# Kernel tuning notes

Measured on AMD Instinct MI355X. Metric: run time of the kernel, lower is better.

The kernel has to match this reference:

```python
import jax, jax.numpy as jnp
import numpy as np

B, T, C_IN, PL, H, W = 8, 8, 256, 64, 56, 56
NT = B * T
RED = 4
CR = PL // RED            # 16 corr feature channels
PS = 7                    # patch size -> 49 correlation channels
KK = PS * PS
EPS = 1e-5
_BN_INV = np.float32(1.0 / np.sqrt(1.0 + EPS))  # eval-mode BN, running_mean=0, running_var=1


def _bn4(x, g, b):  # x [N,C,H,W], per-channel affine (eval-mode BN)
    return x * (g * _BN_INV)[None, :, None, None] + b[None, :, None, None]


def _bn5(x, g, b):  # x [B,T,C,H,W], channel axis 2
    return x * (g * _BN_INV)[None, None, :, None, None] + b[None, None, :, None, None]


def _tconv(x, w):  # depthwise temporal conv: x [B,T,Cq,H,W], w [Cq,K], 'same' padding in T
    K = w.shape[1]
    pad = K // 2
    Tn = x.shape[1]
    xp = jnp.pad(x, ((0, 0), (pad, pad), (0, 0), (0, 0), (0, 0)))
    out = w[:, 0][None, None, :, None, None] * xp[:, 0:Tn]
    for k in range(1, K):
        out = out + w[:, k][None, None, :, None, None] * xp[:, k:k + Tn]
    return out


def _correlation(a, b):  # SpatialCorrelationSampler(kernel=1, patch=PS): a,b [N,C,h,w] -> [N,PS*PS,h,w]
    pad = PS // 2
    h, w = a.shape[2], a.shape[3]
    bp = jnp.pad(b, ((0, 0), (0, 0), (pad, pad), (pad, pad)))
    outs = [jnp.sum(a * bp[:, :, di:di + h, dj:dj + w], axis=1)
            for di in range(PS) for dj in range(PS)]
    return jnp.stack(outs, axis=1)


def setup_inputs() -> dict:
    key = jax.random.key(0)
    ks = jax.random.split(key, 24)
    r = lambda i, shape, s: jax.random.normal(ks[i], shape, dtype=jnp.float32) * s
    return {
        "x": jax.random.normal(ks[0], (NT, C_IN, H, W), dtype=jnp.float32),
        "w1": r(1, (C_IN // 4, 1), 0.3), "w3": r(2, (C_IN // 4, 3), 0.3),
        "w5": r(3, (C_IN // 4, 5), 0.3), "w7": r(4, (C_IN // 4, 7), 0.3),
        "w_conv1": r(5, (PL, C_IN), 0.05), "g1": 1.0 + r(6, (PL,), 0.1), "b1": r(7, (PL,), 0.1),
        "w_conv21": r(8, (CR, PL), 0.1), "g21": 1.0 + r(9, (CR,), 0.1), "b21": r(10, (CR,), 0.1),
        "g22": 1.0 + r(11, (KK,), 0.1), "b22": r(12, (KK,), 0.1),
        "w_conv22": r(13, (PL, KK), 0.1), "g23": 1.0 + r(14, (PL,), 0.1), "b23": r(15, (PL,), 0.1),
        "w_conv2": r(16, (PL, PL, 3, 3), 0.05), "g2": 1.0 + r(17, (PL,), 0.1), "b2": r(18, (PL,), 0.1),
        "w_conv3": r(19, (C_IN, PL), 0.05), "g3": 1.0 + r(20, (C_IN,), 0.1), "b3": r(21, (C_IN,), 0.1),
    }


def reference(x, w1, w3, w5, w7, w_conv1, g1, b1, w_conv21, g21, b21,
              g22, b22, w_conv22, g23, b23, w_conv2, g2, b2, w_conv3, g3, b3):
    residual = x  # stride=1, no downsample
    # ms_group: split channels in 4 quarters, temporal dw conv k=1/3/5/7
    xt = x.reshape(B, T, C_IN, H, W)
    q = C_IN // 4
    parts = [_tconv(xt[:, :, i * q:(i + 1) * q], w) for i, w in enumerate((w1, w3, w5, w7))]
    out = jnp.concatenate(parts, axis=2).reshape(NT, C_IN, H, W)
    # net.conv1 (1x1) + bn1 + relu
    out = jax.nn.relu(_bn4(jnp.einsum('nchw,oc->nohw', out, w_conv1), g1, b1))
    # corr_outer
    res2 = out
    yt = out.reshape(B, T, PL, H, W)
    y = jax.nn.relu(_bn5(jnp.einsum('btchw,oc->btohw', yt, w_conv21), g21, b21))  # conv21+bn21
    idx = jnp.concatenate([jnp.arange(1, T), jnp.array([T - 1])])  # next-frame shift
    y2 = y[:, idx]
    a = y.reshape(NT, CR, H, W)
    b_ = y2.reshape(NT, CR, H, W)
    corr = _correlation(a, b_) / CR                         # [NT,49,H,W]
    corr = jax.nn.relu(_bn4(corr, g22, b22))
    out2 = jax.nn.relu(_bn4(jnp.einsum('nkhw,ok->nohw', corr, w_conv22), g23, b23) + res2)
    # net.conv2 (3x3) + bn2 + relu
    out = jax.lax.conv_general_dilated(out, w_conv2, (1, 1), 'SAME',
                                       dimension_numbers=('NCHW', 'OIHW', 'NCHW'))
    out = jax.nn.relu(_bn4(out, g2, b2))
    out = out + out2
    # net.conv3 (1x1) + bn3 + residual + relu
    out = _bn4(jnp.einsum('nchw,oc->nohw', out, w_conv3), g3, b3) + residual
    return jax.nn.relu(out)
```

## Files before the change

### kernel.cpp

```cpp
#include <hip/hip_runtime.h>


#define MSC_BNI 0.9999950000374997f

typedef __attribute__((ext_vector_type(8))) short bf16x8;
typedef __attribute__((ext_vector_type(4))) float f32x4;
struct __align__(8) ush4 { unsigned short v[4]; };

static __device__ __forceinline__ float b2f(unsigned short h) {
  return __uint_as_float(((unsigned int)h) << 16);
}
static __device__ __forceinline__ unsigned short f2b(float f) {
  unsigned int u = __float_as_uint(f);
  u = u + 0x7FFFu + ((u >> 16) & 1u);
  return (unsigned short)(u >> 16);
}

__global__ __launch_bounds__(256) void k0_prep(
    const float* w1, const float* w2, const float* w3, const float* w22,
    const float* w21,
    unsigned short* Wt1f, unsigned short* Wt2f, unsigned short* Wt3f,
    unsigned short* Wt4f, unsigned short* Wt5f) {
  int idx = blockIdx.x * 256 + threadIdx.x;
  if (idx < 36864) {
    int j = idx;
    int e = j & 7;
    int lane = (j >> 3) & 63;
    int m = (j >> 9) & 3;
    int kc = (j >> 11) & 1;
    int tap = j >> 12;
    int o = m * 16 + (lane & 15);
    int c = kc * 32 + (lane >> 4) * 8 + e;
    Wt2f[j] = f2b(w2[(o * 64 + c) * 9 + tap]);
  } else if (idx < 36864 + 16384) {
    int j = idx - 36864;
    int e = j & 7;
    int lane = (j >> 3) & 63;
    int m = (j >> 9) & 15;
    int kc = j >> 13;
    int o = m * 16 + (lane & 15);
    int c = kc * 32 + (lane >> 4) * 8 + e;
    Wt3f[j] = f2b(w3[o * 64 + c]);
  } else if (idx < 36864 + 16384 + 16384) {
    int j = idx - 36864 - 16384;
    int e = j & 7;
    int lane = (j >> 3) & 63;
    int m = (j >> 9) & 3;
    int kc = j >> 11;
    int o = m * 16 + (lane & 15);
    int c = kc * 32 + (lane >> 4) * 8 + e;
    Wt1f[j] = f2b(w1[o * 256 + c]);
  } else if (idx < 36864 + 16384 + 16384 + 4096) {
    int j = idx - 36864 - 16384 - 16384;
    int e = j & 7;
    int lane = (j >> 3) & 63;
    int m = (j >> 9) & 3;
    int kc = j >> 11;
    int o = m * 16 + (lane & 15);
    int c = kc * 32 + (lane >> 4) * 8 + e;
    Wt4f[j] = (c < 49) ? f2b(w22[o * 49 + c]) : (unsigned short)0;
  } else if (idx < 36864 + 16384 + 16384 + 4096 + 1024) {
    int j = idx - 36864 - 16384 - 16384 - 4096;
    int e = j & 7;
    int lane = (j >> 3) & 63;
    int kc = j >> 9;
    int o = lane & 15;
    int c = kc * 32 + (lane >> 4) * 8 + e;
    Wt5f[j] = f2b(w21[o * 64 + c]);
  }
}

__global__ __launch_bounds__(256, 2) void k12_fused(
    const float* x, unsigned short* R2t, float* Yt,
    const unsigned short* Wt1f, const unsigned short* Wt5f,
    const float* w1, const float* w3, const float* w5, const float* w7,
    const float* g, const float* bb, const float* g21, const float* b21) {
  __shared__ unsigned short sA[8960];
  int b = blockIdx.x / 98;
  int hw0 = (blockIdx.x % 98) * 32;
  int tid = threadIdx.x;
  int l = tid & 63, wv = tid >> 6;
  int l15 = l & 15, l4 = l >> 4;
  f32x4 acc[2][4][2];
#pragma unroll
  for (int tt = 0; tt < 2; tt++)
#pragma unroll
    for (int m = 0; m < 4; m++)
#pragma unroll
      for (int nt = 0; nt < 2; nt++) acc[tt][m][nt] = (f32x4){0.f, 0.f, 0.f, 0.f};

  int colp = tid & 31;
  int cbase = tid >> 5;

  for (int kc8 = 0; kc8 < 8; kc8++) {
    int c0 = kc8 * 32;
    int q = kc8 >> 1;
#pragma unroll
    for (int p = 0; p < 4; p++) {
      int c = cbase + p * 8;
      int cq = (kc8 & 1) * 32 + c;
      float wf[7];
#pragma unroll
      for (int k = 0; k < 7; k++) wf[k] = 0.f;
      if (q == 0) { wf[3] = w1[cq]; }
      else if (q == 1) { wf[2] = w3[cq*3]; wf[3] = w3[cq*3+1]; wf[4] = w3[cq*3+2]; }
      else if (q == 2) { wf[1] = w5[cq*5]; wf[2] = w5[cq*5+1]; wf[3] = w5[cq*5+2]; wf[4] = w5[cq*5+3]; wf[5] = w5[cq*5+4]; }
      else { wf[0] = w7[cq*7]; wf[1] = w7[cq*7+1]; wf[2] = w7[cq*7+2]; wf[3] = w7[cq*7+3]; wf[4] = w7[cq*7+4]; wf[5] = w7[cq*7+5]; wf[6] = w7[cq*7+6]; }
      const float* xb = x + ((size_t)(b * 8) * 256 + c0 + c) * 3136 + hw0 + colp;
      float xin[8];
#pragma unroll
      for (int t = 0; t < 8; t++) xin[t] = xb[t * 256 * 3136];
#pragma unroll
      for (int t = 0; t < 8; t++) {
        float a = 0.f;
#pragma unroll
        for (int d = -3; d <= 3; d++) {
          int ts = t + d;
          if (ts >= 0 && ts < 8) a = fmaf(wf[d + 3], xin[ts], a);
        }
        sA[(t * 32 + colp) * 34 + c] = f2b(a);
      }
    }
    __syncthreads();
#pragma unroll
    for (int tt = 0; tt < 2; tt++) {
      int t = wv * 2 + tt;
#pragma unroll
      for (int nt = 0; nt < 2; nt++) {
        int colt = nt * 16 + l15;
        bf16x8 bfr = *(const bf16x8*)(sA + (t * 32 + colt) * 34 + l4 * 8);
#pragma unroll
        for (int m = 0; m < 4; m++) {
          bf16x8 a = *(const bf16x8*)(Wt1f + (((kc8 * 4 + m) * 64 + l) << 3));
          acc[tt][m][nt] = __builtin_amdgcn_mfma_f32_16x16x32_bf16(a, bfr, acc[tt][m][nt], 0, 0, 0);
        }
      }
    }
    __syncthreads();
  }
  unsigned short* sOutT = sA;
  for (int tt = 0; tt < 2; tt++) {
#pragma unroll
    for (int m = 0; m < 4; m++)
#pragma unroll
      for (int nt = 0; nt < 2; nt++) {
        int col = nt * 16 + l15;
#pragma unroll
        for (int r = 0; r < 4; r++) {
          int o = m * 16 + l4 * 4 + r;
          float v = fmaxf(fmaf(acc[tt][m][nt][r], g[o] * MSC_BNI, bb[o]), 0.f);
          sOutT[(wv * 32 + col) * 70 + o] = f2b(v);
        }
      }
    __syncthreads();
#pragma unroll
    for (int k = 0; k < 4; k++) {
      int ch = tid + k * 256;
      int tb = ch >> 8, col = (ch >> 3) & 31, gg = ch & 7;
      int t = tb * 2 + tt;
      bf16x8 v = *(const bf16x8*)(sOutT + (tb * 32 + col) * 70 + gg * 8);
      *(bf16x8*)(R2t + (((size_t)(b * 8 + t) * 3136) + hw0 + col) * 64 + gg * 8) = v;
    }
    {
      int t = wv * 2 + tt;
#pragma unroll
      for (int ct2 = 0; ct2 < 2; ct2++) {
        f32x4 a5 = (f32x4){0.f, 0.f, 0.f, 0.f};
#pragma unroll
        for (int kc = 0; kc < 2; kc++) {
          bf16x8 bfr = *(const bf16x8*)(sOutT + (wv * 32 + ct2 * 16 + l15) * 70 + kc * 32 + l4 * 8);
          bf16x8 a = *(const bf16x8*)(Wt5f + ((kc * 64 + l) << 3));
          a5 = __builtin_amdgcn_mfma_f32_16x16x32_bf16(a, bfr, a5, 0, 0, 0);
        }
        int hw = hw0 + ct2 * 16 + l15;
        float4 yv;
        {
          int o0 = l4 * 4;
          yv.x = fmaxf(fmaf(a5[0], g21[o0+0] * MSC_BNI, b21[o0+0]), 0.f);
          yv.y = fmaxf(fmaf(a5[1], g21[o0+1] * MSC_BNI, b21[o0+1]), 0.f);
          yv.z = fmaxf(fmaf(a5[2], g21[o0+2] * MSC_BNI, b21[o0+2]), 0.f);
          yv.w = fmaxf(fmaf(a5[3], g21[o0+3] * MSC_BNI, b21[o0+3]), 0.f);
        }
        *(float4*)(Yt + (((size_t)(b * 8 + t) * 3136) + hw) * 16 + l4 * 4) = yv;
      }
    }
    __syncthreads();
  }
}

__global__ __launch_bounds__(256, 2) void k4_corr(
    const float* Yt, unsigned short* COt, const float* g, const float* bb) {
  __shared__ float sb[10 * 62 * 20];
  int n = blockIdx.x / 14;
  int h0 = (blockIdx.x % 14) * 4;
  int t = n & 7;
  int n2 = (t < 7) ? n + 1 : n;
  const float* Yb = Yt + (size_t)n2 * 3136 * 16;
  for (int idx = threadIdx.x; idx < 2480; idx += 256) {
    int c4 = idx & 3;
    int pix = idx >> 2;
    int r = pix / 62, cl = pix - r * 62;
    int gr = h0 - 3 + r, gc = cl - 3;
    float4 v = make_float4(0.f, 0.f, 0.f, 0.f);
    if (gr >= 0 && gr < 56 && gc >= 0 && gc < 56)
      v = *(const float4*)(Yb + (gr * 56 + gc) * 16 + c4 * 4);
    *(float4*)&sb[(r * 62 + cl) * 20 + c4 * 4] = v;
  }
  __syncthreads();
  int pos = threadIdx.x;
  if (pos < 224) {
    int hl = pos / 56, wcol = pos - (pos / 56) * 56;
    const float* Ya = Yt + ((size_t)n * 3136 + (h0 + hl) * 56 + wcol) * 16;
    float4 a0 = *(const float4*)(Ya + 0);
    float4 a1 = *(const float4*)(Ya + 4);
    float4 a2 = *(const float4*)(Ya + 8);
    float4 a3 = *(const float4*)(Ya + 12);
    float corr[49];
    for (int di = 0; di < 7; di++) {
      for (int dj = 0; dj < 7; dj++) {
        const float* sp = &sb[((hl + di) * 62 + wcol + dj) * 20];
        float4 b0 = *(const float4*)(sp + 0);
        float4 b1 = *(const float4*)(sp + 4);
        float4 b2 = *(const float4*)(sp + 8);
        float4 b3 = *(const float4*)(sp + 12);
        float s = 0.f;
        s = fmaf(a0.x, b0.x, s); s = fmaf(a0.y, b0.y, s);
        s = fmaf(a0.z, b0.z, s); s = fmaf(a0.w, b0.w, s);
        s = fmaf(a1.x, b1.x, s); s = fmaf(a1.y, b1.y, s);
        s = fmaf(a1.z, b1.z, s); s = fmaf(a1.w, b1.w, s);
        s = fmaf(a2.x, b2.x, s); s = fmaf(a2.y, b2.y, s);
        s = fmaf(a2.z, b2.z, s); s = fmaf(a2.w, b2.w, s);
        s = fmaf(a3.x, b3.x, s); s = fmaf(a3.y, b3.y, s);
        s = fmaf(a3.z, b3.z, s); s = fmaf(a3.w, b3.w, s);
        int k = di * 7 + dj;
        corr[k] = fmaxf(fmaf(s * 0.0625f, g[k] * MSC_BNI, bb[k]), 0.f);
      }
    }
    unsigned short* Cp = COt + ((size_t)n * 3136 + (h0 + hl) * 56 + wcol) * 64;
#pragma unroll
    for (int gq = 0; gq < 8; gq++) {
      bf16x8 pv;
#pragma unroll
      for (int j = 0; j < 8; j++) {
        int k = gq * 8 + j;
        pv[j] = (k < 49) ? (short)f2b(corr[k]) : (short)0;
      }
      *(bf16x8*)(Cp + gq * 8) = pv;
    }
  }
}

__global__ __launch_bounds__(256, 2) void k56_mfma(
    const unsigned short* R2t, const unsigned short* COt, unsigned short* C2t,
    const unsigned short* Wt2f, const unsigned short* Wt4f,
    const float* g2, const float* b2, const float* g23, const float* b23) {
  __shared__ unsigned short sIn[22272];
  int n = blockIdx.x / 14;
  int h0 = (blockIdx.x % 14) * 4;
  const unsigned short* Rt = R2t + (size_t)n * 3136 * 64;
  for (int ch = threadIdx.x; ch < 2784; ch += 256) {
    int rc = ch >> 3;
    int cg = ch & 7;
    int row = rc / 58, col = rc - row * 58;
    int gr = h0 - 1 + row, gc = col - 1;
    bf16x8 v = (bf16x8){0, 0, 0, 0, 0, 0, 0, 0};
    if (gr >= 0 && gr < 56 && gc >= 0 && gc < 56)
      v = *(const bf16x8*)(Rt + (gr * 56 + gc) * 64 + cg * 8);
    *(bf16x8*)(sIn + rc * 64 + ((cg ^ (col & 7)) << 3)) = v;
  }
  __syncthreads();
  int l = threadIdx.x & 63;
  int wv = threadIdx.x >> 6;
  int l15 = l & 15, l4 = l >> 4;
  f32x4 acc[4][4];
#pragma unroll
  for (int m = 0; m < 4; m++)
#pragma unroll
    for (int t = 0; t < 4; t++) acc[m][t] = (f32x4){0.f, 0.f, 0.f, 0.f};

  for (int tap = 0; tap < 9; tap++) {
    int ky = tap / 3;
    int kx = tap - ky * 3;
    for (int kc = 0; kc < 2; kc++) {
      bf16x8 a[4];
#pragma unroll
      for (int m = 0; m < 4; m++)
        a[m] = *(const bf16x8*)(Wt2f + ((((tap * 2 + kc) * 4 + m) * 64 + l) << 3));
#pragma unroll
      for (int t = 0; t < 4; t++) {
        int ct = wv * 4 + t;
        int rowt = ct >> 2, col0 = (ct & 3) << 4;
        int lcol = col0 + l15 + kx;
        if (lcol > 57) lcol = 57;
        int us = ((((rowt + ky) * 58 + lcol) * 64) + kc * 32 + (l4 << 3))
                 ^ ((lcol & 7) << 3);
        bf16x8 b = *(const bf16x8*)(sIn + us);
#pragma unroll
        for (int m = 0; m < 4; m++)
          acc[m][t] = __builtin_amdgcn_mfma_f32_16x16x32_bf16(a[m], b, acc[m][t], 0, 0, 0);
      }
    }
  }

#pragma unroll
  for (int t = 0; t < 4; t++) {
    int ct = wv * 4 + t;
    int rowt = ct >> 2, col0 = (ct & 3) << 4;
    int cc = col0 + l15;
    int cc_cl = (cc < 56) ? cc : 55;
    int gbase = ((int)(n * 3136) + (h0 + rowt) * 56 + cc_cl) * 64;
    f32x4 acc2[4];
#pragma unroll
    for (int m = 0; m < 4; m++) acc2[m] = (f32x4){0.f, 0.f, 0.f, 0.f};
#pragma unroll
    for (int kc = 0; kc < 2; kc++) {
      bf16x8 bco = *(const bf16x8*)(COt + gbase + kc * 32 + l4 * 8);
#pragma unroll
      for (int m = 0; m < 4; m++) {
        bf16x8 a = *(const bf16x8*)(Wt4f + (((kc * 4 + m) * 64 + l) << 3));
        acc2[m] = __builtin_amdgcn_mfma_f32_16x16x32_bf16(a, bco, acc2[m], 0, 0, 0);
      }
    }
    if (cc < 56) {
      int rc = (rowt + 1) * 58 + cc + 1;
#pragma unroll
      for (int m = 0; m < 4; m++) {
        int cg0 = 2 * m + (l4 >> 1);
        int us = rc * 64 + ((cg0 ^ ((cc + 1) & 7)) << 3) + (l4 & 1) * 4;
        ush4 rv = *(const ush4*)(sIn + us);
        ush4 ov;
#pragma unroll
        for (int r = 0; r < 4; r++) {
          int o = m * 16 + l4 * 4 + r;
          float o2 = fmaxf(fmaf(acc2[m][r], g23[o] * MSC_BNI, b23[o]) + b2f(rv.v[r]), 0.f);
          float v = fmaxf(fmaf(acc[m][t][r], g2[o] * MSC_BNI, b2[o]), 0.f) + o2;
          ov.v[r] = f2b(v);
        }
        *(ush4*)(C2t + gbase + m * 16 + l4 * 4) = ov;
      }
    }
  }
}

__global__ __launch_bounds__(256, 3) void k7_mfma(
    const unsigned short* C2t, const float* x, float* outp,
    const unsigned short* Wt3f, const float* g, const float* bb) {
  __shared__ float sOut[64 * 68];
  int n = blockIdx.x / 49;
  int hw0 = (blockIdx.x % 49) * 64;
  int l = threadIdx.x & 63;
  int wv = threadIdx.x >> 6;
  int l15 = l & 15, l4 = l >> 4;
  f32x4 acc[4][4];
#pragma unroll
  for (int m = 0; m < 4; m++)
#pragma unroll
    for (int t = 0; t < 4; t++) acc[m][t] = (f32x4){0.f, 0.f, 0.f, 0.f};

#pragma unroll
  for (int kc = 0; kc < 2; kc++) {
    bf16x8 a[4];
#pragma unroll
    for (int m = 0; m < 4; m++)
      a[m] = *(const bf16x8*)(Wt3f + (((kc * 16 + wv * 4 + m) * 64 + l) << 3));
#pragma unroll
    for (int t = 0; t < 4; t++) {
      int colt = t * 16 + l15;
      bf16x8 b = *(const bf16x8*)(C2t + ((size_t)n * 3136 + hw0 + colt) * 64 + kc * 32 + l4 * 8);
#pragma unroll
      for (int m = 0; m < 4; m++)
        acc[m][t] = __builtin_amdgcn_mfma_f32_16x16x32_bf16(a[m], b, acc[m][t], 0, 0, 0);
    }
  }

  for (int m = 0; m < 4; m++) {
#pragma unroll
    for (int t = 0; t < 4; t++)
#pragma unroll
      for (int r = 0; r < 4; r++)
        sOut[(wv * 16 + l4 * 4 + r) * 68 + t * 16 + l15] = acc[m][t][r];
    __syncthreads();
#pragma unroll
    for (int s = 0; s < 4; s++) {
      int ro = (threadIdx.x >> 4) + s * 16;
      int o = (ro >> 4) * 64 + m * 16 + (ro & 15);
      int colq = (threadIdx.x & 15) * 4;
      float4 v = *(float4*)&sOut[ro * 68 + colq];
      int off = (n * 256 + o) * 3136 + hw0 + colq;
      float4 xv = *(const float4*)(x + off);
      float sg = g[o] * MSC_BNI, bo = bb[o];
      float4 ov;
      ov.x = fmaxf(fmaf(v.x, sg, bo) + xv.x, 0.f);
      ov.y = fmaxf(fmaf(v.y, sg, bo) + xv.y, 0.f);
      ov.z = fmaxf(fmaf(v.z, sg, bo) + xv.z, 0.f);
      ov.w = fmaxf(fmaf(v.w, sg, bo) + xv.w, 0.f);
      *(float4*)(outp + off) = ov;
    }
    __syncthreads();
  }
}

extern "C" void kernel_launch(void* const* d_in, const int* in_sizes, int n_in,
                              void* d_out, int out_size, void* d_ws, size_t ws_size,
                              hipStream_t stream) {
  const float* x        = (const float*)d_in[0];
  const float* w1       = (const float*)d_in[1];
  const float* w3       = (const float*)d_in[2];
  const float* w5       = (const float*)d_in[3];
  const float* w7       = (const float*)d_in[4];
  const float* w_conv1  = (const float*)d_in[5];
  const float* g1       = (const float*)d_in[6];
  const float* b1       = (const float*)d_in[7];
  const float* w_conv21 = (const float*)d_in[8];
  const float* g21      = (const float*)d_in[9];
  const float* b21      = (const float*)d_in[10];
  const float* g22      = (const float*)d_in[11];
  const float* b22      = (const float*)d_in[12];
  const float* w_conv22 = (const float*)d_in[13];
  const float* g23      = (const float*)d_in[14];
  const float* b23      = (const float*)d_in[15];
  const float* w_conv2  = (const float*)d_in[16];
  const float* g2       = (const float*)d_in[17];
  const float* b2       = (const float*)d_in[18];
  const float* w_conv3  = (const float*)d_in[19];
  const float* g3       = (const float*)d_in[20];
  const float* b3       = (const float*)d_in[21];

  char* ob = (char*)d_out;
  char* ws = (char*)d_ws;
  float*          Yt   = (float*)ob;
  unsigned short* COt  = (unsigned short*)(ob + 12845056);
  unsigned short* R2t  = (unsigned short*)(ob + 103563264);
  unsigned short* Wt2f = (unsigned short*)(ob + 134217728);
  unsigned short* Wt1f = (unsigned short*)(ob + 134291456);
  unsigned short* Wt4f = (unsigned short*)(ob + 134324224);
  unsigned short* Wt5f = (unsigned short*)(ob + 134332416);
  unsigned short* C2t  = (unsigned short*)ws;
  unsigned short* Wt3f = (unsigned short*)(ws + 25690112);

  k0_prep  <<<dim3(292),     dim3(256), 0, stream>>>(w_conv1, w_conv2, w_conv3, w_conv22,
                                                     w_conv21, Wt1f, Wt2f, Wt3f, Wt4f, Wt5f);
  k12_fused<<<dim3(8 * 98),  dim3(256), 0, stream>>>(x, R2t, Yt, Wt1f, Wt5f,
                                                     w1, w3, w5, w7, g1, b1, g21, b21);
  k4_corr  <<<dim3(64 * 14), dim3(256), 0, stream>>>(Yt, COt, g22, b22);
  k56_mfma <<<dim3(64 * 14), dim3(256), 0, stream>>>(R2t, COt, C2t, Wt2f, Wt4f, g2, b2, g23, b23);
  k7_mfma  <<<dim3(64 * 49), dim3(256), 0, stream>>>(C2t, x, (float*)d_out, Wt3f, g3, b3);
}
```

Measured before the change: 250.1 us.

## Double-buffer LDS and prefetch next channel chunk during MFMA in fused conv1 kernel

The fused temporal-conv plus conv1 kernel now double-buffers its LDS tile. Global loads of x and the temporal weights for chunk k+1 are issued before the MFMA loop on chunk k, and the next buffer is filled afterwards. This removes one barrier per iteration and is meant to hide global load latency behind the matrix math. In exchange, LDS use doubles (about 34KB per block) and the prefetched values add registers, which could cut occupancy below the 2 blocks/SM launch bound.

```diff
diff --git a/kernel.cpp b/kernel.cpp
--- a/kernel.cpp
+++ b/kernel.cpp
@@ -75,60 +75,81 @@
     const unsigned short* Wt1f, const unsigned short* Wt5f,
     const float* w1, const float* w3, const float* w5, const float* w7,
     const float* g, const float* bb, const float* g21, const float* b21) {
-  __shared__ unsigned short sA[8960];
+  __shared__ unsigned short lds[17408];
   int b = blockIdx.x / 98;
   int hw0 = (blockIdx.x % 98) * 32;
   int tid = threadIdx.x;
   int l = tid & 63, wv = tid >> 6;
   int l15 = l & 15, l4 = l >> 4;
-  f32x4 acc[2][4][2];
-#pragma unroll
-  for (int tt = 0; tt < 2; tt++)
-#pragma unroll
-    for (int m = 0; m < 4; m++)
-#pragma unroll
-      for (int nt = 0; nt < 2; nt++) acc[tt][m][nt] = (f32x4){0.f, 0.f, 0.f, 0.f};
-
   int colp = tid & 31;
   int cbase = tid >> 5;
+  const int tstr = 256 * 3136;
+
+  f32x4 acc[2][4][2];
+#pragma unroll
+  for (int tt = 0; tt < 2; tt++)
+#pragma unroll
+    for (int m = 0; m < 4; m++)
+#pragma unroll
+      for (int nt = 0; nt < 2; nt++) acc[tt][m][nt] = (f32x4){0.f, 0.f, 0.f, 0.f};
+
+  float xn[4][8];
+  float wfn[4][7];
+
+#pragma unroll
+  for (int p = 0; p < 4; p++) {
+    int c = cbase + p * 8;
+    const float* xb = x + ((size_t)(b * 8) * 256 + c) * 3136 + hw0 + colp;
+#pragma unroll
+    for (int t = 0; t < 8; t++) xn[p][t] = xb[t * tstr];
+#pragma unroll
+    for (int k = 0; k < 7; k++) wfn[p][k] = 0.f;
+    wfn[p][3] = w1[c];
+  }
+#pragma unroll
+  for (int p = 0; p < 4; p++) {
+    int c = cbase + p * 8;
+#pragma unroll
+    for (int t = 0; t < 8; t++) {
+      float a = 0.f;
+#pragma unroll
+      for (int d = -3; d <= 3; d++) {
+        int ts = t + d;
+        if (ts >= 0 && ts < 8) a = fmaf(wfn[p][d + 3], xn[p][ts], a);
+      }
+      lds[(t * 32 + colp) * 34 + c] = f2b(a);
+    }
+  }
 
   for (int kc8 = 0; kc8 < 8; kc8++) {
-    int c0 = kc8 * 32;
-    int q = kc8 >> 1;
-#pragma unroll
-    for (int p = 0; p < 4; p++) {
-      int c = cbase + p * 8;
-      int cq = (kc8 & 1) * 32 + c;
-      float wf[7];
-#pragma unroll
-      for (int k = 0; k < 7; k++) wf[k] = 0.f;
-      if (q == 0) { wf[3] = w1[cq]; }
-      else if (q == 1) { wf[2] = w3[cq*3]; wf[3] = w3[cq*3+1]; wf[4] = w3[cq*3+2]; }
-      else if (q == 2) { wf[1] = w5[cq*5]; wf[2] = w5[cq*5+1]; wf[3] = w5[cq*5+2]; wf[4] = w5[cq*5+3]; wf[5] = w5[cq*5+4]; }
-      else { wf[0] = w7[cq*7]; wf[1] = w7[cq*7+1]; wf[2] = w7[cq*7+2]; wf[3] = w7[cq*7+3]; wf[4] = w7[cq*7+4]; wf[5] = w7[cq*7+5]; wf[6] = w7[cq*7+6]; }
-      const float* xb = x + ((size_t)(b * 8) * 256 + c0 + c) * 3136 + hw0 + colp;
-      float xin[8];
-#pragma unroll
-      for (int t = 0; t < 8; t++) xin[t] = xb[t * 256 * 3136];
-#pragma unroll
-      for (int t = 0; t < 8; t++) {
-        float a = 0.f;
-#pragma unroll
-        for (int d = -3; d <= 3; d++) {
-          int ts = t + d;
-          if (ts >= 0 && ts < 8) a = fmaf(wf[d + 3], xin[ts], a);
-        }
-        sA[(t * 32 + colp) * 34 + c] = f2b(a);
-      }
-    }
     __syncthreads();
+    unsigned short* bufc = lds + (kc8 & 1) * 8704;
+    unsigned short* bufn = lds + ((kc8 + 1) & 1) * 8704;
+    if (kc8 < 7) {
+      int kn = kc8 + 1;
+      int qn = kn >> 1;
+#pragma unroll
+      for (int p = 0; p < 4; p++) {
+        int c = cbase + p * 8;
+        const float* xb = x + ((size_t)(b * 8) * 256 + kn * 32 + c) * 3136 + hw0 + colp;
+#pragma unroll
+        for (int t = 0; t < 8; t++) xn[p][t] = xb[t * tstr];
+        int cq = (kn & 1) * 32 + c;
+#pragma unroll
+        for (int k = 0; k < 7; k++) wfn[p][k] = 0.f;
+        if (qn == 0) { wfn[p][3] = w1[cq]; }
+        else if (qn == 1) { wfn[p][2] = w3[cq*3]; wfn[p][3] = w3[cq*3+1]; wfn[p][4] = w3[cq*3+2]; }
+        else if (qn == 2) { wfn[p][1] = w5[cq*5]; wfn[p][2] = w5[cq*5+1]; wfn[p][3] = w5[cq*5+2]; wfn[p][4] = w5[cq*5+3]; wfn[p][5] = w5[cq*5+4]; }
+        else { wfn[p][0] = w7[cq*7]; wfn[p][1] = w7[cq*7+1]; wfn[p][2] = w7[cq*7+2]; wfn[p][3] = w7[cq*7+3]; wfn[p][4] = w7[cq*7+4]; wfn[p][5] = w7[cq*7+5]; wfn[p][6] = w7[cq*7+6]; }
+      }
+    }
 #pragma unroll
     for (int tt = 0; tt < 2; tt++) {
       int t = wv * 2 + tt;
 #pragma unroll
       for (int nt = 0; nt < 2; nt++) {
         int colt = nt * 16 + l15;
-        bf16x8 bfr = *(const bf16x8*)(sA + (t * 32 + colt) * 34 + l4 * 8);
+        bf16x8 bfr = *(const bf16x8*)(bufc + (t * 32 + colt) * 34 + l4 * 8);
 #pragma unroll
         for (int m = 0; m < 4; m++) {
           bf16x8 a = *(const bf16x8*)(Wt1f + (((kc8 * 4 + m) * 64 + l) << 3));
@@ -136,9 +157,25 @@
         }
       }
     }
-    __syncthreads();
-  }
-  unsigned short* sOutT = sA;
+    if (kc8 < 7) {
+#pragma unroll
+      for (int p = 0; p < 4; p++) {
+        int c = cbase + p * 8;
+#pragma unroll
+        for (int t = 0; t < 8; t++) {
+          float a = 0.f;
+#pragma unroll
+          for (int d = -3; d <= 3; d++) {
+            int ts = t + d;
+            if (ts >= 0 && ts < 8) a = fmaf(wfn[p][d + 3], xn[p][ts], a);
+          }
+          bufn[(t * 32 + colp) * 34 + c] = f2b(a);
+        }
+      }
+    }
+  }
+  __syncthreads();
+  unsigned short* sOutT = lds;
   for (int tt = 0; tt < 2; tt++) {
 #pragma unroll
     for (int m = 0; m < 4; m++)
```

Measured after the change: 238.5 us. -4.7%, faster.

## Double-buffer temporal-conv staging in fused conv1 kernel and raise occupancy bounds

Applied to the files above, without the earlier changes.

The fused temporal-shift plus conv1 kernel now keeps two LDS buffers and prefetches the next x channel chunks into registers while MFMAs consume the current buffer. This is meant to hide the global load latency behind matrix work instead of serialising load, convert and compute. It doubles LDS use and adds register pressure for the prefetch arrays. Separately, the launch bounds of the correlation and conv2 kernels are raised to target three blocks per SIMD, which could cause spills.

```diff
diff --git a/kernel.cpp b/kernel.cpp
--- a/kernel.cpp
+++ b/kernel.cpp
@@ -75,60 +75,73 @@
     const unsigned short* Wt1f, const unsigned short* Wt5f,
     const float* w1, const float* w3, const float* w5, const float* w7,
     const float* g, const float* bb, const float* g21, const float* b21) {
-  __shared__ unsigned short sA[8960];
+  __shared__ unsigned short lds[17408];
   int b = blockIdx.x / 98;
   int hw0 = (blockIdx.x % 98) * 32;
   int tid = threadIdx.x;
   int l = tid & 63, wv = tid >> 6;
   int l15 = l & 15, l4 = l >> 4;
-  f32x4 acc[2][4][2];
-#pragma unroll
-  for (int tt = 0; tt < 2; tt++)
-#pragma unroll
-    for (int m = 0; m < 4; m++)
-#pragma unroll
-      for (int nt = 0; nt < 2; nt++) acc[tt][m][nt] = (f32x4){0.f, 0.f, 0.f, 0.f};
-
   int colp = tid & 31;
   int cbase = tid >> 5;
-
-  for (int kc8 = 0; kc8 < 8; kc8++) {
-    int c0 = kc8 * 32;
-    int q = kc8 >> 1;
+  const int tstr = 256 * 3136;
+
+  f32x4 acc[2][4][2];
+#pragma unroll
+  for (int tt = 0; tt < 2; tt++)
+#pragma unroll
+    for (int m = 0; m < 4; m++)
+#pragma unroll
+      for (int nt = 0; nt < 2; nt++) acc[tt][m][nt] = (f32x4){0.f, 0.f, 0.f, 0.f};
+
+  float xnA[4][8], xnB[4][8], wfc[4][7];
+
+  auto loadx = [&](int kn, float xv[4][8]) {
 #pragma unroll
     for (int p = 0; p < 4; p++) {
       int c = cbase + p * 8;
-      int cq = (kc8 & 1) * 32 + c;
-      float wf[7];
-#pragma unroll
-      for (int k = 0; k < 7; k++) wf[k] = 0.f;
-      if (q == 0) { wf[3] = w1[cq]; }
-      else if (q == 1) { wf[2] = w3[cq*3]; wf[3] = w3[cq*3+1]; wf[4] = w3[cq*3+2]; }
-      else if (q == 2) { wf[1] = w5[cq*5]; wf[2] = w5[cq*5+1]; wf[3] = w5[cq*5+2]; wf[4] = w5[cq*5+3]; wf[5] = w5[cq*5+4]; }
-      else { wf[0] = w7[cq*7]; wf[1] = w7[cq*7+1]; wf[2] = w7[cq*7+2]; wf[3] = w7[cq*7+3]; wf[4] = w7[cq*7+4]; wf[5] = w7[cq*7+5]; wf[6] = w7[cq*7+6]; }
-      const float* xb = x + ((size_t)(b * 8) * 256 + c0 + c) * 3136 + hw0 + colp;
-      float xin[8];
-#pragma unroll
-      for (int t = 0; t < 8; t++) xin[t] = xb[t * 256 * 3136];
+      const float* xb = x + ((size_t)(b * 8) * 256 + kn * 32 + c) * 3136 + hw0 + colp;
+#pragma unroll
+      for (int t = 0; t < 8; t++) xv[p][t] = xb[t * tstr];
+    }
+  };
+  auto loadwf = [&](int kn) {
+    int qn = kn >> 1;
+#pragma unroll
+    for (int p = 0; p < 4; p++) {
+      int c = cbase + p * 8;
+      int cq = (kn & 1) * 32 + c;
+#pragma unroll
+      for (int k = 0; k < 7; k++) wfc[p][k] = 0.f;
+      if (qn == 0) { wfc[p][3] = w1[cq]; }
+      else if (qn == 1) { wfc[p][2] = w3[cq*3]; wfc[p][3] = w3[cq*3+1]; wfc[p][4] = w3[cq*3+2]; }
+      else if (qn == 2) { wfc[p][1] = w5[cq*5]; wfc[p][2] = w5[cq*5+1]; wfc[p][3] = w5[cq*5+2]; wfc[p][4] = w5[cq*5+3]; wfc[p][5] = w5[cq*5+4]; }
+      else { wfc[p][0] = w7[cq*7]; wfc[p][1] = w7[cq*7+1]; wfc[p][2] = w7[cq*7+2]; wfc[p][3] = w7[cq*7+3]; wfc[p][4] = w7[cq*7+4]; wfc[p][5] = w7[cq*7+5]; wfc[p][6] = w7[cq*7+6]; }
+    }
+  };
+  auto tconv = [&](const float xv[4][8], unsigned short* buf) {
+#pragma unroll
+    for (int p = 0; p < 4; p++) {
+      int c = cbase + p * 8;
 #pragma unroll
       for (int t = 0; t < 8; t++) {
         float a = 0.f;
 #pragma unroll
         for (int d = -3; d <= 3; d++) {
           int ts = t + d;
-          if (ts >= 0 && ts < 8) a = fmaf(wf[d + 3], xin[ts], a);
-        }
-        sA[(t * 32 + colp) * 34 + c] = f2b(a);
-      }
-    }
-    __syncthreads();
+          if (ts >= 0 && ts < 8) a = fmaf(wfc[p][d + 3], xv[p][ts], a);
+        }
+        buf[(t * 32 + colp) * 34 + c] = f2b(a);
+      }
+    }
+  };
+  auto mfma_step = [&](const unsigned short* buf, int kc8) {
 #pragma unroll
     for (int tt = 0; tt < 2; tt++) {
       int t = wv * 2 + tt;
 #pragma unroll
       for (int nt = 0; nt < 2; nt++) {
         int colt = nt * 16 + l15;
-        bf16x8 bfr = *(const bf16x8*)(sA + (t * 32 + colt) * 34 + l4 * 8);
+        bf16x8 bfr = *(const bf16x8*)(buf + (t * 32 + colt) * 34 + l4 * 8);
 #pragma unroll
         for (int m = 0; m < 4; m++) {
           bf16x8 a = *(const bf16x8*)(Wt1f + (((kc8 * 4 + m) * 64 + l) << 3));
@@ -136,9 +149,27 @@
         }
       }
     }
-    __syncthreads();
-  }
-  unsigned short* sOutT = sA;
+  };
+
+  loadx(0, xnA);
+  loadx(1, xnB);
+  loadwf(0);
+  tconv(xnA, lds);
+
+#pragma unroll
+  for (int kk = 0; kk < 8; kk += 2) {
+    __syncthreads();
+    if (kk + 2 < 8) loadx(kk + 2, xnA);
+    mfma_step(lds, kk);
+    loadwf(kk + 1);
+    tconv(xnB, lds + 8704);
+    __syncthreads();
+    if (kk + 3 < 8) loadx(kk + 3, xnB);
+    mfma_step(lds + 8704, kk + 1);
+    if (kk + 2 < 8) { loadwf(kk + 2); tconv(xnA, lds); }
+  }
+  __syncthreads();
+  unsigned short* sOutT = lds;
   for (int tt = 0; tt < 2; tt++) {
 #pragma unroll
     for (int m = 0; m < 4; m++)
@@ -188,7 +219,7 @@
   }
 }
 
-__global__ __launch_bounds__(256, 2) void k4_corr(
+__global__ __launch_bounds__(256, 3) void k4_corr(
     const float* Yt, unsigned short* COt, const float* g, const float* bb) {
   __shared__ float sb[10 * 62 * 20];
   int n = blockIdx.x / 14;
@@ -250,7 +281,7 @@
   }
 }
 
-__global__ __launch_bounds__(256, 2) void k56_mfma(
+__global__ __launch_bounds__(256, 3) void k56_mfma(
     const unsigned short* R2t, const unsigned short* COt, unsigned short* C2t,
     const unsigned short* Wt2f, const unsigned short* Wt4f,
     const float* g2, const float* b2, const float* g23, const float* b23) {
```

Measured after the change: 228.9 us (median of 2 runs). 1.09x faster.

## Split fused temporal-conv+conv1 kernel into separate tconv and MFMA GEMM kernels

Applied to the files above, without the earlier changes.

Unfuses the temporal depthwise conv from the conv1 GEMM. A new elementwise kernel writes the bf16 tconv output to an intermediate buffer in global memory. A separate MFMA kernel then loads a 256-channel by 64-pixel tile into swizzled LDS and computes conv1 and conv21 with far more blocks. The goal is better parallelism and coalesced vectorized x reads, paid for with an extra round trip of roughly 100MB through global memory. Launch bounds for the corr and conv2 kernels are raised to 3 blocks per CU.

```diff
diff --git a/kernel.cpp b/kernel.cpp
--- a/kernel.cpp
+++ b/kernel.cpp
@@ -70,125 +70,115 @@
   }
 }
 
-__global__ __launch_bounds__(256, 2) void k12_fused(
-    const float* x, unsigned short* R2t, float* Yt,
+__global__ __launch_bounds__(256, 8) void k1_tconv(
+    const float* x, unsigned short* A,
+    const float* w1, const float* w3, const float* w5, const float* w7) {
+  int i = blockIdx.x * 256 + threadIdx.x;
+  int hw4 = i % 784;
+  int bc = i / 784;
+  int c = bc & 255;
+  int b = bc >> 8;
+  int q = c >> 6, cc = c & 63;
+  float wf[7];
+#pragma unroll
+  for (int k = 0; k < 7; k++) wf[k] = 0.f;
+  if (q == 0) { wf[3] = w1[cc]; }
+  else if (q == 1) { wf[2] = w3[cc*3]; wf[3] = w3[cc*3+1]; wf[4] = w3[cc*3+2]; }
+  else if (q == 2) { wf[1] = w5[cc*5]; wf[2] = w5[cc*5+1]; wf[3] = w5[cc*5+2]; wf[4] = w5[cc*5+3]; wf[5] = w5[cc*5+4]; }
+  else { wf[0] = w7[cc*7]; wf[1] = w7[cc*7+1]; wf[2] = w7[cc*7+2]; wf[3] = w7[cc*7+3]; wf[4] = w7[cc*7+4]; wf[5] = w7[cc*7+5]; wf[6] = w7[cc*7+6]; }
+
+  const float4* xp = (const float4*)x;
+  size_t base = ((size_t)(b * 8) * 256 + c) * 784 + hw4;
+  const int tstr = 256 * 784;
+  float4 xv[8];
+#pragma unroll
+  for (int t = 0; t < 8; t++) xv[t] = xp[base + t * tstr];
+#pragma unroll
+  for (int t = 0; t < 8; t++) {
+    float4 a = make_float4(0.f, 0.f, 0.f, 0.f);
+#pragma unroll
+    for (int d = -3; d <= 3; d++) {
+      int ts = t + d;
+      if (ts >= 0 && ts < 8) {
+        float wvv = wf[d + 3];
+        a.x = fmaf(wvv, xv[ts].x, a.x);
+        a.y = fmaf(wvv, xv[ts].y, a.y);
+        a.z = fmaf(wvv, xv[ts].z, a.z);
+        a.w = fmaf(wvv, xv[ts].w, a.w);
+      }
+    }
+    ush4 ov;
+    ov.v[0] = f2b(a.x); ov.v[1] = f2b(a.y); ov.v[2] = f2b(a.z); ov.v[3] = f2b(a.w);
+    *(ush4*)(A + (((size_t)(b * 8 + t) * 256 + c) * 3136 + hw4 * 4)) = ov;
+  }
+}
+
+__global__ __launch_bounds__(256, 2) void k2_mfma(
+    const unsigned short* A, unsigned short* R2t, float* Yt,
     const unsigned short* Wt1f, const unsigned short* Wt5f,
-    const float* w1, const float* w3, const float* w5, const float* w7,
     const float* g, const float* bb, const float* g21, const float* b21) {
-  __shared__ unsigned short sA[8960];
-  int b = blockIdx.x / 98;
-  int hw0 = (blockIdx.x % 98) * 32;
-  int tid = threadIdx.x;
-  int l = tid & 63, wv = tid >> 6;
+  __shared__ unsigned short sA[16384];
+  __shared__ unsigned short sOutT[64 * 70];
+  int n = blockIdx.x / 49;
+  int hw0 = (blockIdx.x % 49) * 64;
+  const unsigned short* Ab = A + (size_t)n * 256 * 3136 + hw0;
+  for (int idx = threadIdx.x; idx < 16384; idx += 256) {
+    int c = idx >> 6, col = idx & 63;
+    sA[(col * 256 + c) ^ ((col & 7) << 3)] = Ab[c * 3136 + col];
+  }
+  __syncthreads();
+  int l = threadIdx.x & 63;
+  int wv = threadIdx.x >> 6;
   int l15 = l & 15, l4 = l >> 4;
-  f32x4 acc[2][4][2];
-#pragma unroll
-  for (int tt = 0; tt < 2; tt++)
-#pragma unroll
-    for (int m = 0; m < 4; m++)
-#pragma unroll
-      for (int nt = 0; nt < 2; nt++) acc[tt][m][nt] = (f32x4){0.f, 0.f, 0.f, 0.f};
-
-  int colp = tid & 31;
-  int cbase = tid >> 5;
-
-  for (int kc8 = 0; kc8 < 8; kc8++) {
-    int c0 = kc8 * 32;
-    int q = kc8 >> 1;
-#pragma unroll
-    for (int p = 0; p < 4; p++) {
-      int c = cbase + p * 8;
-      int cq = (kc8 & 1) * 32 + c;
-      float wf[7];
-#pragma unroll
-      for (int k = 0; k < 7; k++) wf[k] = 0.f;
-      if (q == 0) { wf[3] = w1[cq]; }
-      else if (q == 1) { wf[2] = w3[cq*3]; wf[3] = w3[cq*3+1]; wf[4] = w3[cq*3+2]; }
-      else if (q == 2) { wf[1] = w5[cq*5]; wf[2] = w5[cq*5+1]; wf[3] = w5[cq*5+2]; wf[4] = w5[cq*5+3]; wf[5] = w5[cq*5+4]; }
-      else { wf[0] = w7[cq*7]; wf[1] = w7[cq*7+1]; wf[2] = w7[cq*7+2]; wf[3] = w7[cq*7+3]; wf[4] = w7[cq*7+4]; wf[5] = w7[cq*7+5]; wf[6] = w7[cq*7+6]; }
-      const float* xb = x + ((size_t)(b * 8) * 256 + c0 + c) * 3136 + hw0 + colp;
-      float xin[8];
-#pragma unroll
-      for (int t = 0; t < 8; t++) xin[t] = xb[t * 256 * 3136];
-#pragma unroll
-      for (int t = 0; t < 8; t++) {
-        float a = 0.f;
-#pragma unroll
-        for (int d = -3; d <= 3; d++) {
-          int ts = t + d;
-          if (ts >= 0 && ts < 8) a = fmaf(wf[d + 3], xin[ts], a);
-        }
-        sA[(t * 32 + colp) * 34 + c] = f2b(a);
-      }
-    }
-    __syncthreads();
-#pragma unroll
-    for (int tt = 0; tt < 2; tt++) {
-      int t = wv * 2 + tt;
-#pragma unroll
-      for (int nt = 0; nt < 2; nt++) {
-        int colt = nt * 16 + l15;
-        bf16x8 bfr = *(const bf16x8*)(sA + (t * 32 + colt) * 34 + l4 * 8);
-#pragma unroll
-        for (int m = 0; m < 4; m++) {
-          bf16x8 a = *(const bf16x8*)(Wt1f + (((kc8 * 4 + m) * 64 + l) << 3));
-          acc[tt][m][nt] = __builtin_amdgcn_mfma_f32_16x16x32_bf16(a, bfr, acc[tt][m][nt], 0, 0, 0);
-        }
-      }
-    }
-    __syncthreads();
-  }
-  unsigned short* sOutT = sA;
-  for (int tt = 0; tt < 2; tt++) {
-#pragma unroll
-    for (int m = 0; m < 4; m++)
-#pragma unroll
-      for (int nt = 0; nt < 2; nt++) {
-        int col = nt * 16 + l15;
-#pragma unroll
-        for (int r = 0; r < 4; r++) {
-          int o = m * 16 + l4 * 4 + r;
-          float v = fmaxf(fmaf(acc[tt][m][nt][r], g[o] * MSC_BNI, bb[o]), 0.f);
-          sOutT[(wv * 32 + col) * 70 + o] = f2b(v);
-        }
-      }
-    __syncthreads();
-#pragma unroll
-    for (int k = 0; k < 4; k++) {
-      int ch = tid + k * 256;
-      int tb = ch >> 8, col = (ch >> 3) & 31, gg = ch & 7;
-      int t = tb * 2 + tt;
-      bf16x8 v = *(const bf16x8*)(sOutT + (tb * 32 + col) * 70 + gg * 8);
-      *(bf16x8*)(R2t + (((size_t)(b * 8 + t) * 3136) + hw0 + col) * 64 + gg * 8) = v;
-    }
-    {
-      int t = wv * 2 + tt;
-#pragma unroll
-      for (int ct2 = 0; ct2 < 2; ct2++) {
-        f32x4 a5 = (f32x4){0.f, 0.f, 0.f, 0.f};
-#pragma unroll
-        for (int kc = 0; kc < 2; kc++) {
-          bf16x8 bfr = *(const bf16x8*)(sOutT + (wv * 32 + ct2 * 16 + l15) * 70 + kc * 32 + l4 * 8);
-          bf16x8 a = *(const bf16x8*)(Wt5f + ((kc * 64 + l) << 3));
-          a5 = __builtin_amdgcn_mfma_f32_16x16x32_bf16(a, bfr, a5, 0, 0, 0);
-        }
-        int hw = hw0 + ct2 * 16 + l15;
-        float4 yv;
-        {
-          int o0 = l4 * 4;
-          yv.x = fmaxf(fmaf(a5[0], g21[o0+0] * MSC_BNI, b21[o0+0]), 0.f);
-          yv.y = fmaxf(fmaf(a5[1], g21[o0+1] * MSC_BNI, b21[o0+1]), 0.f);
-          yv.z = fmaxf(fmaf(a5[2], g21[o0+2] * MSC_BNI, b21[o0+2]), 0.f);
-          yv.w = fmaxf(fmaf(a5[3], g21[o0+3] * MSC_BNI, b21[o0+3]), 0.f);
-        }
-        *(float4*)(Yt + (((size_t)(b * 8 + t) * 3136) + hw) * 16 + l4 * 4) = yv;
-      }
-    }
-    __syncthreads();
-  }
-}
-
-__global__ __launch_bounds__(256, 2) void k4_corr(
+  f32x4 acc[4];
+#pragma unroll
+  for (int m = 0; m < 4; m++) acc[m] = (f32x4){0.f, 0.f, 0.f, 0.f};
+#pragma unroll
+  for (int kc = 0; kc < 8; kc++) {
+    int colt = wv * 16 + l15;
+    int us = (colt * 256 + kc * 32 + (l4 << 3)) ^ ((colt & 7) << 3);
+    bf16x8 b = *(const bf16x8*)(sA + us);
+#pragma unroll
+    for (int m = 0; m < 4; m++) {
+      bf16x8 a = *(const bf16x8*)(Wt1f + (((kc * 4 + m) * 64 + l) << 3));
+      acc[m] = __builtin_amdgcn_mfma_f32_16x16x32_bf16(a, b, acc[m], 0, 0, 0);
+    }
+  }
+  int colw = wv * 16 + l15;
+#pragma unroll
+  for (int m = 0; m < 4; m++) {
+#pragma unroll
+    for (int r = 0; r < 4; r++) {
+      int o = m * 16 + l4 * 4 + r;
+      float v = fmaxf(fmaf(acc[m][r], g[o] * MSC_BNI, bb[o]), 0.f);
+      sOutT[colw * 70 + o] = f2b(v);
+    }
+  }
+  __syncthreads();
+#pragma unroll
+  for (int k = 0; k < 2; k++) {
+    int ch = threadIdx.x + k * 256;
+    int col = ch >> 3, gg = ch & 7;
+    bf16x8 v = *(const bf16x8*)(sOutT + col * 70 + gg * 8);
+    *(bf16x8*)(R2t + ((size_t)n * 3136 + hw0 + col) * 64 + gg * 8) = v;
+  }
+  f32x4 a5 = (f32x4){0.f, 0.f, 0.f, 0.f};
+#pragma unroll
+  for (int kc = 0; kc < 2; kc++) {
+    bf16x8 bfr = *(const bf16x8*)(sOutT + colw * 70 + kc * 32 + l4 * 8);
+    bf16x8 a = *(const bf16x8*)(Wt5f + ((kc * 64 + l) << 3));
+    a5 = __builtin_amdgcn_mfma_f32_16x16x32_bf16(a, bfr, a5, 0, 0, 0);
+  }
+  int o0 = l4 * 4;
+  float4 yv;
+  yv.x = fmaxf(fmaf(a5[0], g21[o0+0] * MSC_BNI, b21[o0+0]), 0.f);
+  yv.y = fmaxf(fmaf(a5[1], g21[o0+1] * MSC_BNI, b21[o0+1]), 0.f);
+  yv.z = fmaxf(fmaf(a5[2], g21[o0+2] * MSC_BNI, b21[o0+2]), 0.f);
+  yv.w = fmaxf(fmaf(a5[3], g21[o0+3] * MSC_BNI, b21[o0+3]), 0.f);
+  *(float4*)(Yt + ((size_t)n * 3136 + hw0 + colw) * 16 + o0) = yv;
+}
+
+__global__ __launch_bounds__(256, 3) void k4_corr(
     const float* Yt, unsigned short* COt, const float* g, const float* bb) {
   __shared__ float sb[10 * 62 * 20];
   int n = blockIdx.x / 14;
@@ -250,7 +240,7 @@
   }
 }
 
-__global__ __launch_bounds__(256, 2) void k56_mfma(
+__global__ __launch_bounds__(256, 3) void k56_mfma(
     const unsigned short* R2t, const unsigned short* COt, unsigned short* C2t,
     const unsigned short* Wt2f, const unsigned short* Wt4f,
     const float* g2, const float* b2, const float* g23, const float* b23) {
@@ -429,20 +419,22 @@
   char* ob = (char*)d_out;
   char* ws = (char*)d_ws;
   float*          Yt   = (float*)ob;
+  unsigned short* A    = (unsigned short*)(ob + 12845056);
   unsigned short* COt  = (unsigned short*)(ob + 12845056);
-  unsigned short* R2t  = (unsigned short*)(ob + 103563264);
-  unsigned short* Wt2f = (unsigned short*)(ob + 134217728);
-  unsigned short* Wt1f = (unsigned short*)(ob + 134291456);
-  unsigned short* Wt4f = (unsigned short*)(ob + 134324224);
-  unsigned short* Wt5f = (unsigned short*)(ob + 134332416);
+  unsigned short* R2t  = (unsigned short*)(ob + 115605504);
+  unsigned short* Wt2f = (unsigned short*)(ob + 141295616);
+  unsigned short* Wt1f = (unsigned short*)(ob + 141369344);
+  unsigned short* Wt4f = (unsigned short*)(ob + 141402112);
+  unsigned short* Wt5f = (unsigned short*)(ob + 141410304);
   unsigned short* C2t  = (unsigned short*)ws;
   unsigned short* Wt3f = (unsigned short*)(ws + 25690112);
 
-  k0_prep  <<<dim3(292),     dim3(256), 0, stream>>>(w_conv1, w_conv2, w_conv3, w_conv22,
-                                                     w_conv21, Wt1f, Wt2f, Wt3f, Wt4f, Wt5f);
-  k12_fused<<<dim3(8 * 98),  dim3(256), 0, stream>>>(x, R2t, Yt, Wt1f, Wt5f,
-                                                     w1, w3, w5, w7, g1, b1, g21, b21);
-  k4_corr  <<<dim3(64 * 14), dim3(256), 0, stream>>>(Yt, COt, g22, b22);
-  k56_mfma <<<dim3(64 * 14), dim3(256), 0, stream>>>(R2t, COt, C2t, Wt2f, Wt4f, g2, b2, g23, b23);
-  k7_mfma  <<<dim3(64 * 49), dim3(256), 0, stream>>>(C2t, x, (float*)d_out, Wt3f, g3, b3);
-}
+  k0_prep <<<dim3(292),     dim3(256), 0, stream>>>(w_conv1, w_conv2, w_conv3, w_conv22,
+                                                    w_conv21, Wt1f, Wt2f, Wt3f, Wt4f, Wt5f);
+  k1_tconv<<<dim3(6272),    dim3(256), 0, stream>>>(x, A, w1, w3, w5, w7);
+  k2_mfma <<<dim3(64 * 49), dim3(256), 0, stream>>>(A, R2t, Yt, Wt1f, Wt5f,
+                                                    g1, b1, g21, b21);
+  k4_corr <<<dim3(64 * 14), dim3(256), 0, stream>>>(Yt, COt, g22, b22);
+  k56_mfma<<<dim3(64 * 14), dim3(256), 0, stream>>>(R2t, COt, C2t, Wt2f, Wt4f, g2, b2, g23, b23);
+  k7_mfma <<<dim3(64 * 49), dim3(256), 0, stream>>>(C2t, x, (float*)d_out, Wt3f, g3, b3);
+}
```

Measured after the change: 263.1 us. 5.2% more time.
